# Performance work log

Hardware: AMD Instinct MI355X
Metric: run time of the kernel (lower is better)

## Reference

```python
import jax, jax.numpy as jnp
import numpy as np

B, L, H, W = 16, 4096, 64, 64
SEQ = 1024  # target_sequence_length (hardcoded in the torch module)
SP = 32     # sqrt(SEQ)


def _conv1d(x, w, b, pad):
    y = jax.lax.conv_general_dilated(x, w, (1,), [(pad, pad)],
                                     dimension_numbers=('NCH', 'OIH', 'NCH'))
    return y + b[None, :, None]


def _conv2d(x, w, b, pad, groups=1):
    y = jax.lax.conv_general_dilated(x, w, (1, 1), [(pad, pad)] * 2,
                                     feature_group_count=groups,
                                     dimension_numbers=('NCHW', 'OIHW', 'NCHW'))
    return y + b[None, :, None, None]


def _forward(us_input, img_input, us_w1, us_b1, us_w2, us_b2, us_w3, us_b3,
             aff_w, aff_w_high, aff_thr, img_w1, img_b1, img_w2, img_b2, img_w3, img_b3,
             db_qkv_w, db_qkv_b, db_dw_w, db_dw_b, db_proj_w, db_proj_b,
             db_fc_w, db_fc_b, db_dep_w, db_dep_b, db_temp,
             ca_qkv_w, ca_qkv_b, ca_out_w, ca_out_b,
             tf_ch1_w, tf_ch1_b, tf_ch2_w, tf_ch2_b,
             tf_sp1_w, tf_sp1_b, tf_sp2_w, tf_sp2_b, cls_w, cls_b):
    b = us_input.shape[0]
    # ---- ultrasound 1D conv branch ----
    x = us_input.transpose(0, 2, 1)                    # [B,1,L]
    x = jax.nn.relu(_conv1d(x, us_w1, us_b1, 1))
    x = jax.nn.relu(_conv1d(x, us_w2, us_b2, 1))
    x = jax.nn.relu(_conv1d(x, us_w3, us_b3, 1))
    us_feat = x.transpose(0, 2, 1)                     # [B,L,64]
    # ---- adaptive frequency filtering (training-mode high-freq mask included) ----
    n = us_feat.shape[1]
    xf = jnp.fft.rfft(us_feat, axis=1, norm='ortho')   # [B,Nf,64] complex
    w_c = aff_w[:, 0] + 1j * aff_w[:, 1]
    xw = xf * w_c
    energy = jnp.sum(jnp.abs(xf) ** 2, axis=-1)        # [B,Nf]
    med = jnp.median(energy.reshape(b, -1), axis=1, keepdims=True)
    ne = energy / (med + 1e-6)
    hard = (ne > aff_thr).astype(jnp.float32)
    mask = jax.lax.stop_gradient(hard - aff_thr) + aff_thr  # straight-through threshold
    wh_c = aff_w_high[:, 0] + 1j * aff_w_high[:, 1]
    xw = xw + (xf * mask[..., None]) * wh_c
    us_feat = jnp.fft.irfft(xw, n=n, axis=1, norm='ortho')  # [B,L,64]
    # ---- image 2D conv branch ----
    y = jax.nn.relu(_conv2d(img_input, img_w1, img_b1, 1))
    y = jax.nn.relu(_conv2d(y, img_w2, img_b2, 1))
    y = jax.nn.relu(_conv2d(y, img_w3, img_b3, 1))     # [B,64,H,W]
    # ---- dual-branch feature fusion block ----
    hgt, wid = y.shape[2], y.shape[3]
    hw = hgt * wid
    qkv = jnp.einsum('oi,bihw->bohw', db_qkv_w, y) + db_qkv_b[None, :, None, None]
    qkv = _conv2d(qkv, db_dw_w, db_dw_b, 1, groups=192)      # depthwise (3x3x3 conv @ D=1 -> center 3x3)
    # convolutional branch: faithful row-major reshape as in torch
    f_all = qkv.reshape(b, hw, 12, 16).transpose(0, 2, 1, 3)  # [B,12,HW,16]
    f_all = jnp.einsum('oi,bink->bonk', db_fc_w, f_all) + db_fc_b[None, :, None, None]
    f_conv = f_all.transpose(0, 3, 1, 2).reshape(b, 144, hgt, wid)
    out_conv = _conv2d(f_conv, db_dep_w, db_dep_b, 1, groups=16)  # [B,64,H,W]
    # channel attention branch
    q, k, v = jnp.split(qkv, 3, axis=1)
    q = q.reshape(b, 4, 16, hw)
    k = k.reshape(b, 4, 16, hw)
    v = v.reshape(b, 4, 16, hw)
    q = q / jnp.maximum(jnp.linalg.norm(q, axis=-1, keepdims=True), 1e-12)
    k = k / jnp.maximum(jnp.linalg.norm(k, axis=-1, keepdims=True), 1e-12)
    attn = jax.nn.softmax(jnp.einsum('bhcn,bhdn->bhcd', q, k) * db_temp, axis=-1)
    out = jnp.einsum('bhcd,bhdn->bhcn', attn, v).reshape(b, 64, hgt, wid)
    out = jnp.einsum('oi,bihw->bohw', db_proj_w, out) + db_proj_b[None, :, None, None]
    img_feat = (out + out_conv).reshape(b, 64, hw).transpose(0, 2, 1)  # [B,HW,64]
    # ---- adaptive avg pool to SEQ (lengths divide evenly) ----
    us_red = us_feat.transpose(0, 2, 1).reshape(b, 64, SEQ, -1).mean(-1).transpose(0, 2, 1)
    img_red = img_feat.transpose(0, 2, 1).reshape(b, 64, SEQ, -1).mean(-1).transpose(0, 2, 1)
    # ---- cross-modal attention (shared qkv/out projections) ----
    def heads(t):
        u = (jnp.einsum('bli,oi->blo', t, ca_qkv_w) + ca_qkv_b).reshape(b, SEQ, 4, 3, 16)
        return (u[:, :, :, 0].transpose(0, 2, 1, 3),
                u[:, :, :, 1].transpose(0, 2, 1, 3),
                u[:, :, :, 2].transpose(0, 2, 1, 3))
    q1, k1, v1 = heads(us_red)
    q2, k2, v2 = heads(img_red)
    scale = 1.0 / jnp.sqrt(jnp.float32(16.0))
    a1 = jax.nn.softmax(jnp.einsum('bhqd,bhkd->bhqk', q1, k2) * scale, axis=-1)
    a2 = jax.nn.softmax(jnp.einsum('bhqd,bhkd->bhqk', q2, k1) * scale, axis=-1)
    o1 = jnp.einsum('bhqk,bhkd->bhqd', a1, v2).transpose(0, 2, 1, 3).reshape(b, SEQ, 64)
    o2 = jnp.einsum('bhqk,bhkd->bhqd', a2, v1).transpose(0, 2, 1, 3).reshape(b, SEQ, 64)
    o1 = jnp.einsum('bli,oi->blo', o1, ca_out_w) + ca_out_b
    o2 = jnp.einsum('bli,oi->blo', o2, ca_out_w) + ca_out_b
    t1 = o1.transpose(0, 2, 1).reshape(b, 64, SP, SP)
    t2 = o2.transpose(0, 2, 1).reshape(b, 64, SP, SP)
    # ---- modal fusion attention (channel + spatial gating) ----
    ch_pool = jnp.stack([t1.mean((2, 3)), t1.max((2, 3)), t2.mean((2, 3)), t2.max((2, 3))], axis=1)  # [B,4,64]
    c1 = _conv1d(ch_pool, tf_ch1_w, tf_ch1_b, 1)      # [B,1,64]
    c2 = _conv1d(ch_pool, tf_ch2_w, tf_ch2_b, 1)
    ch_stack = jax.nn.softmax(jnp.stack([c1, c2], 0), axis=0)      # [2,B,1,64]
    ch_stack = ch_stack.transpose(0, 1, 3, 2)[..., None]           # [2,B,64,1,1]
    sp_pool = jnp.concatenate([t1.mean(1, keepdims=True), t1.max(1, keepdims=True),
                               t2.mean(1, keepdims=True), t2.max(1, keepdims=True)], axis=1)
    s1 = _conv2d(sp_pool, tf_sp1_w, tf_sp1_b, 3)
    s2 = _conv2d(sp_pool, tf_sp2_w, tf_sp2_b, 3)
    sp_stack = jax.nn.softmax(jnp.stack([s1, s2], 0), axis=0)      # [2,B,1,SP,SP]
    att = ch_stack + sp_stack + 1.0                                # [2,B,64,SP,SP]
    fuse = att[0] * t1 + att[1] * t2
    logits = fuse.mean((2, 3)) @ cls_w.T + cls_b
    return jax.nn.softmax(logits, axis=1)


def setup_inputs() -> dict:
    key = jax.random.key(0)
    ks = iter(jax.random.split(key, 64))
    def rn(shape, s=0.2):
        return jax.random.normal(next(ks), shape, dtype=jnp.float32) * s
    d = {
        'us_input': jax.random.normal(next(ks), (B, L, 1), dtype=jnp.float32),
        'img_input': jax.random.normal(next(ks), (B, 3, H, W), dtype=jnp.float32),
        'us_w1': rn((16, 1, 3)), 'us_b1': rn((16,), 0.02),
        'us_w2': rn((32, 16, 3)), 'us_b2': rn((32,), 0.02),
        'us_w3': rn((64, 32, 3)), 'us_b3': rn((64,), 0.02),
        'aff_w': rn((64, 2), 0.02), 'aff_w_high': rn((64, 2), 0.02),
        'aff_thr': jax.random.uniform(next(ks), (1,), dtype=jnp.float32),
        'img_w1': rn((16, 3, 3, 3)), 'img_b1': rn((16,), 0.02),
        'img_w2': rn((32, 16, 3, 3)), 'img_b2': rn((32,), 0.02),
        'img_w3': rn((64, 32, 3, 3)), 'img_b3': rn((64,), 0.02),
        'db_qkv_w': rn((192, 64), 0.1), 'db_qkv_b': rn((192,), 0.02),
        'db_dw_w': rn((192, 1, 3, 3)), 'db_dw_b': rn((192,), 0.02),
        'db_proj_w': rn((64, 64), 0.1), 'db_proj_b': rn((64,), 0.02),
        'db_fc_w': rn((9, 12), 0.1), 'db_fc_b': rn((9,), 0.02),
        'db_dep_w': rn((64, 9, 3, 3), 0.1), 'db_dep_b': rn((64,), 0.02),
        'db_temp': jnp.ones((4, 1, 1), dtype=jnp.float32),
        'ca_qkv_w': rn((192, 64), 0.1), 'ca_qkv_b': rn((192,), 0.02),
        'ca_out_w': rn((64, 64), 0.1), 'ca_out_b': rn((64,), 0.02),
        'tf_ch1_w': rn((1, 4, 3)), 'tf_ch1_b': rn((1,), 0.02),
        'tf_ch2_w': rn((1, 4, 3)), 'tf_ch2_b': rn((1,), 0.02),
        'tf_sp1_w': rn((1, 4, 7, 7)), 'tf_sp1_b': rn((1,), 0.02),
        'tf_sp2_w': rn((1, 4, 7, 7)), 'tf_sp2_b': rn((1,), 0.02),
        'cls_w': rn((9, 64), 0.1), 'cls_b': rn((9,), 0.02),
    }
    return d


def reference(us_input, img_input, us_w1, us_b1, us_w2, us_b2, us_w3, us_b3,
              aff_w, aff_w_high, aff_thr, img_w1, img_b1, img_w2, img_b2, img_w3, img_b3,
              db_qkv_w, db_qkv_b, db_dw_w, db_dw_b, db_proj_w, db_proj_b,
              db_fc_w, db_fc_b, db_dep_w, db_dep_b, db_temp,
              ca_qkv_w, ca_qkv_b, ca_out_w, ca_out_b,
              tf_ch1_w, tf_ch1_b, tf_ch2_w, tf_ch2_b,
              tf_sp1_w, tf_sp1_b, tf_sp2_w, tf_sp2_b, cls_w, cls_b):
    return _forward(us_input, img_input, us_w1, us_b1, us_w2, us_b2, us_w3, us_b3,
                    aff_w, aff_w_high, aff_thr, img_w1, img_b1, img_w2, img_b2, img_w3, img_b3,
                    db_qkv_w, db_qkv_b, db_dw_w, db_dw_b, db_proj_w, db_proj_b,
                    db_fc_w, db_fc_b, db_dep_w, db_dep_b, db_temp,
                    ca_qkv_w, ca_qkv_b, ca_out_w, ca_out_b,
                    tf_ch1_w, tf_ch1_b, tf_ch2_w, tf_ch2_b,
                    tf_sp1_w, tf_sp1_b, tf_sp2_w, tf_sp2_b, cls_w, cls_b)
```

## Files before the change

### kernel.cpp

```cpp
#include <hip/hip_runtime.h>

typedef float v2f __attribute__((ext_vector_type(2)));

static constexpr size_t O_SMALL   = 0;
static constexpr size_t O_US3     = 3145728;
static constexpr size_t O_XF      = 7340032;
static constexpr size_t O_USFILT  = 11536384;
static constexpr size_t O_ENERGY  = 15730688;
static constexpr size_t O_MED     = 15764480;
static constexpr size_t O_NRM     = 15765504;
static constexpr size_t O_ATTNS   = 15767552;
static constexpr size_t O_CHPOOL  = 15783936;
static constexpr size_t O_CHW     = 15788032;
static constexpr size_t O_SPPOOL  = 15790080;
static constexpr size_t O_SPW     = 15855616;
static constexpr size_t O_QKV     = 15888384;
static constexpr size_t O_QKVDW   = 28471296;
static constexpr size_t O_OUTCONV = 41054208;
static constexpr size_t CA_USRED = 0, CA_IMGRED = 1, CA_Q1 = 2, CA_K1 = 3, CA_V1 = 4,
                        CA_Q2 = 5, CA_K2 = 6, CA_V2 = 7, CA_O1 = 8, CA_O2 = 9,
                        CA_T1 = 10, CA_T2 = 11;

template<int Ci, int Co>
__global__ __launch_bounds__(256) void conv1d3_t(const float* __restrict__ in,
    const float* __restrict__ w, const float* __restrict__ bs, float* __restrict__ out)
{
    constexpr int T = 128;
    constexpr int G = 256 / Co;
    constexpr int N = T / G;
    __shared__ float lds[Ci][T + 2];
    int tid = threadIdx.x;
    int b  = blockIdx.x >> 5;
    int t0 = (blockIdx.x & 31) * T;
    const float* inb = in + (size_t)b * Ci * 4096;
    for (int i = tid; i < Ci * T; i += 256) {
        int ci = i / T, x = i % T;
        lds[ci][x + 1] = inb[ci * 4096 + t0 + x];
    }
    if (tid < Ci) {
        lds[tid][0]     = (t0 > 0)        ? inb[tid * 4096 + t0 - 1] : 0.f;
        lds[tid][T + 1] = (t0 + T < 4096) ? inb[tid * 4096 + t0 + T] : 0.f;
    }
    __syncthreads();
    int co = tid / G;
    int x0 = (tid % G) * N;
    float acc[N];
    float bias = bs[co];
#pragma unroll
    for (int j = 0; j < N; ++j) acc[j] = bias;
    const float* wb = w + co * Ci * 3;
    for (int ci = 0; ci < Ci; ++ci) {
        float w0 = wb[ci * 3], w1 = wb[ci * 3 + 1], w2 = wb[ci * 3 + 2];
        float a = lds[ci][x0], bb = lds[ci][x0 + 1];
#pragma unroll
        for (int j = 0; j < N; ++j) {
            float cc = lds[ci][x0 + 2 + j];
            acc[j] += w0 * a + w1 * bb + w2 * cc;
            a = bb; bb = cc;
        }
    }
    float* ob = out + ((size_t)b * Co + co) * 4096 + t0 + x0;
#pragma unroll
    for (int j = 0; j < N; ++j) ob[j] = fmaxf(acc[j], 0.f);
}

template<int Ci, int Co, int TY>
__global__ __launch_bounds__(256) void conv2d3_t(const float* __restrict__ in,
    const float* __restrict__ w, const float* __restrict__ bs, float* __restrict__ out)
{
    constexpr int G = 256 / (Co * TY);
    constexpr int N = 64 / G;
    __shared__ float lds[Ci][TY + 2][66];
    int tid = threadIdx.x;
    constexpr int NB = 64 / TY;
    int b  = blockIdx.x / NB;
    int y0 = (blockIdx.x % NB) * TY;
    const float* inb = in + (size_t)b * Ci * 4096;
    for (int i = tid; i < Ci * (TY + 2) * 64; i += 256) {
        int x  = i & 63;
        int ry = (i >> 6) % (TY + 2);
        int ci = i / ((TY + 2) * 64);
        int gy = y0 - 1 + ry;
        lds[ci][ry][x + 1] = (gy >= 0 && gy < 64) ? inb[ci * 4096 + gy * 64 + x] : 0.f;
    }
    for (int r = tid; r < Ci * (TY + 2); r += 256) {
        int ry = r % (TY + 2), ci = r / (TY + 2);
        lds[ci][ry][0] = 0.f; lds[ci][ry][65] = 0.f;
    }
    __syncthreads();
    int co   = tid / (TY * G);
    int ysub = (tid / G) % TY;
    int x0   = (tid % G) * N;
    float acc[N];
    float bias = bs[co];
#pragma unroll
    for (int j = 0; j < N; ++j) acc[j] = bias;
    const float* wb = w + co * Ci * 9;
    for (int ci = 0; ci < Ci; ++ci) {
        float wr[9];
#pragma unroll
        for (int k = 0; k < 9; ++k) wr[k] = wb[ci * 9 + k];
#pragma unroll
        for (int dy = 0; dy < 3; ++dy) {
            const float* lr = &lds[ci][ysub + dy][x0];
            float a = lr[0], bb = lr[1];
#pragma unroll
            for (int j = 0; j < N; ++j) {
                float cc = lr[2 + j];
                acc[j] += wr[dy * 3] * a + wr[dy * 3 + 1] * bb + wr[dy * 3 + 2] * cc;
// ... 13 lines not shown
    for (int s = 0; s < 6; ++s) {
        float cfac = -0.25f / (float)Ns;
        for (int r = 0; r < 4; ++r) {
            int j = (r << 8) + tid;
            float2 v0 = src[j];
            float2 v1 = src[j + 1024];
            float2 v2 = src[j + 2048];
            float2 v3 = src[j + 3072];
            int jm = j & (Ns - 1);
            float rev = (float)jm * cfac;
            float s1 = __builtin_amdgcn_sinf(rev);
            float c1 = __builtin_amdgcn_cosf(rev);
            float c2 = c1 * c1 - s1 * s1, s2 = 2.f * c1 * s1;
            float c3 = c2 * c1 - s2 * s1, s3 = c2 * s1 + s2 * c1;
            float2 u1 = make_float2(v1.x * c1 - v1.y * s1, v1.x * s1 + v1.y * c1);
            float2 u2 = make_float2(v2.x * c2 - v2.y * s2, v2.x * s2 + v2.y * c2);
            float2 u3 = make_float2(v3.x * c3 - v3.y * s3, v3.x * s3 + v3.y * c3);
            float t0x = v0.x + u2.x, t0y = v0.y + u2.y;
            float t1x = v0.x - u2.x, t1y = v0.y - u2.y;
            float t2x = u1.x + u3.x, t2y = u1.y + u3.y;
            float t3x = u1.x - u3.x, t3y = u1.y - u3.y;
            int base = ((j - jm) << 2) + jm;
            dst[base]          = make_float2(t0x + t2x, t0y + t2y);
            dst[base + Ns]     = make_float2(t1x + t3y, t1y - t3x);
            dst[base + 2 * Ns] = make_float2(t0x - t2x, t0y - t2y);
            dst[base + 3 * Ns] = make_float2(t1x - t3y, t1y + t3x);
        }
        __syncthreads();
        float2* tmp = src; src = dst; dst = tmp;
        Ns <<= 2;
    }
}

__global__ __launch_bounds__(256) void fft_fwd_kernel(const float* __restrict__ us3,
                                                      float* __restrict__ xf)
{
    __shared__ float2 A[4096];
    __shared__ float2 Bb[4096];
    int row = blockIdx.x;
    int tid = threadIdx.x;
    const float* x = us3 + (size_t)row * 4096;
    for (int r = 0; r < 16; ++r) {
        int i = (r << 8) + tid;
        A[i] = make_float2(x[i], 0.f);
    }
    __syncthreads();
    fft4096_r4(A, Bb, tid);
    float* out = xf + (size_t)row * 4098;
    for (int r = 0; r < 9; ++r) {
        int f = (r << 8) + tid;
        if (f < 2049) {
            out[2 * f]     = A[f].x * (1.f / 64.f);
            out[2 * f + 1] = A[f].y * (1.f / 64.f);
        }
    }
}

__global__ __launch_bounds__(256) void energy_kernel(const float* __restrict__ xf,
                                                     float* __restrict__ energy)
{
    int idx = blockIdx.x * 256 + threadIdx.x;
    if (idx >= 16 * 2049) return;
    int b = idx / 2049, f = idx % 2049;
    const float* p = xf + (size_t)b * 64 * 4098 + 2 * f;
    float e = 0.f;
    for (int ch = 0; ch < 64; ++ch) {
        float re = p[0], im = p[1];
        e += re * re + im * im;
        p += 4098;
    }
    energy[idx] = e;
}

__global__ __launch_bounds__(256) void median_kernel(const float* __restrict__ energy,
                                                     float* __restrict__ med)
{
    __shared__ float s[4096];
    int b = blockIdx.x;
    int tid = threadIdx.x;
    for (int r = 0; r < 16; ++r) {
        int i = (r << 8) + tid;
        s[i] = (i < 2049) ? energy[b * 2049 + i] : 3.0e38f;
    }
    __syncthreads();
    for (int k = 2; k <= 4096; k <<= 1) {
        for (int j = k >> 1; j > 0; j >>= 1) {
            for (int r = 0; r < 16; ++r) {
                int i = (r << 8) + tid;
                int ixj = i ^ j;
                if (ixj > i) {
                    bool up = ((i & k) == 0);
                    float a = s[i], bb = s[ixj];
                    if ((a > bb) == up) { s[i] = bb; s[ixj] = a; }
                }
            }
            __syncthreads();
        }
    }
    if (tid == 0) med[b] = s[1024];
}

__global__ __launch_bounds__(256) void filter_ifft_kernel(
    const float* __restrict__ xf, const float* __restrict__ energy, const float* __restrict__ med,
    const float* __restrict__ aff_w, const float* __restrict__ aff_wh, const float* __restrict__ thr_p,
    float* __restrict__ us_filt)
{
    __shared__ float2 A[4096];
    __shared__ float2 Bb[4096];
    int row = blockIdx.x;
    int b = row >> 6, ch = row & 63;
    int tid = threadIdx.x;
    float thr = thr_p[0];
    float mden = med[b] + 1e-6f;
    float w0r = aff_w[2 * ch], w0i = aff_w[2 * ch + 1];
    float whr = aff_wh[2 * ch], whi = aff_wh[2 * ch + 1];
    const float* X = xf + (size_t)row * 4098;
    const float* E = energy + b * 2049;
    for (int r = 0; r < 9; ++r) {
        int f = (r << 8) + tid;
        if (f < 2049) {
            float re = X[2 * f], im = X[2 * f + 1];
            float mask = (E[f] / mden > thr) ? 1.f : 0.f;
            float wr = w0r + mask * whr;
            float wi = w0i + mask * whi;
            float xr = re * wr - im * wi;
            float xi = re * wi + im * wr;
            A[f] = make_float2(xr, -xi);
            if (f >= 1 && f <= 2047) A[4096 - f] = make_float2(xr, xi);
        }
    }
    __syncthreads();
    fft4096_r4(A, Bb, tid);
    float* out = us_filt + (size_t)row * 4096;
    for (int r = 0; r < 16; ++r) {
        int i = (r << 8) + tid;
        out[i] = A[i].x * (1.f / 64.f);
    }
}

__global__ __launch_bounds__(256, 2) void qkv1x1_kernel(const float* __restrict__ y,
    const float* __restrict__ w, const float* __restrict__ bs, float* __restrict__ out)
{
    int blk = blockIdx.x;
    int oc = blk & 3;
    int pc = (blk >> 2) & 15;
    int b  = blk >> 6;
    int p = pc * 256 + threadIdx.x;
    const float* inb = y + (size_t)b * 262144 + p;
    v2f reg[32];
#pragma unroll
    for (int ci = 0; ci < 32; ++ci) {
        v2f r; r.x = inb[(2 * ci) * 4096]; r.y = inb[(2 * ci + 1) * 4096];
        reg[ci] = r;
    }
    float* ob = out + (size_t)b * 786432 + (size_t)oc * 48 * 4096 + p;
    for (int o = 0; o < 48; ++o) {
        const v2f* wr = (const v2f*)(w + (oc * 48 + o) * 64);
        v2f s2 = {0.f, 0.f};
#pragma unroll
        for (int ci = 0; ci < 32; ++ci) s2 = wr[ci] * reg[ci] + s2;
        ob[o * 4096] = bs[oc * 48 + o] + s2.x + s2.y;
    }
}

__global__ __launch_bounds__(256) void dwconv_kernel(const float* __restrict__ in,
    const float* __restrict__ w, const float* __restrict__ bs, float* __restrict__ out)
{
    int idx = blockIdx.x * 256 + threadIdx.x;
    int x = idx & 63, yy = (idx >> 6) & 63;
    int c = (idx >> 12) % 192;
    const float* p = in + idx;
    const float* wp = w + c * 9;
    float acc = bs[c];
    bool ym = yy > 0, yp = yy < 63, xm = x > 0, xp = x < 63;
    float s = wp[4] * p[0];
    if (ym) { s += wp[1] * p[-64]; if (xm) s += wp[0] * p[-65]; if (xp) s += wp[2] * p[-63]; }
    if (xm) s += wp[3] * p[-1];
    if (xp) s += wp[5] * p[1];
    if (yp) { s += wp[7] * p[64];  if (xm) s += wp[6] * p[63];  if (xp) s += wp[8] * p[65]; }
    out[idx] = acc + s;
}

__global__ __launch_bounds__(256) void fc_kernel(const float* __restrict__ qkv_dw,
    const float* __restrict__ fw, const float* __restrict__ fb, float* __restrict__ fcv)
{
    int idx = blockIdx.x * 256 + threadIdx.x;
    int k = idx & 15;
    int p = (idx >> 4) & 4095;
    int b = idx >> 16;
    const float* base = qkv_dw + (size_t)b * 786432;
    float u[12];
#pragma unroll
    for (int i = 0; i < 12; ++i) u[i] = base[p * 192 + i * 16 + k];
#pragma unroll
    for (int o = 0; o < 9; ++o) {
        float s = fb[o];
#pragma unroll
        for (int i = 0; i < 12; ++i) s += fw[o * 12 + i] * u[i];
        fcv[(((size_t)b * 16 + k) * 9 + o) * 4096 + p] = s;
    }
}

__global__ __launch_bounds__(256) void depconv2_kernel(const float* __restrict__ fcv,
    const float* __restrict__ w, const float* __restrict__ bs, float* __restrict__ out)
{
    __shared__ float lds[9][10][66];
    int blk = blockIdx.x;
    int band = blk & 7;
    int g    = (blk >> 3) & 15;
    int b    = blk >> 7;
    int y0 = band * 8;
    int tid = threadIdx.x;
    const float* inb = fcv + ((size_t)(b * 16 + g) * 9) * 4096;
    for (int i = tid; i < 9 * 10 * 64; i += 256) {
        int x  = i & 63;
        int ry = (i >> 6) % 10;
        int ci = i / 640;
        int gy = y0 - 1 + ry;
        lds[ci][ry][x + 1] = (gy >= 0 && gy < 64) ? inb[ci * 4096 + gy * 64 + x] : 0.f;
    }
    for (int i = tid; i < 90; i += 256) {
        int ry = i % 10, ci = i / 10;
        lds[ci][ry][0] = 0.f; lds[ci][ry][65] = 0.f;
    }
    __syncthreads();
    int co   = tid >> 6;
    int ysub = (tid >> 3) & 7;
    int x0   = (tid & 7) * 8;
    int ocg  = g * 4 + co;
    float acc[8];
    float bias = bs[ocg];
#pragma unroll
    for (int j = 0; j < 8; ++j) acc[j] = bias;
    const float* wb = w + ocg * 81;
    for (int ci = 0; ci < 9; ++ci) {
        float wr[9];
#pragma unroll
        for (int k = 0; k < 9; ++k) wr[k] = wb[ci * 9 + k];
#pragma unroll
        for (int dy = 0; dy < 3; ++dy) {
            const float* lr = &lds[ci][ysub + dy][x0];
            float a = lr[0], bb = lr[1];
#pragma unroll
            for (int j = 0; j < 8; ++j) {
                float cc = lr[2 + j];
                acc[j] += wr[dy * 3] * a + wr[dy * 3 + 1] * bb + wr[dy * 3 + 2] * cc;
                a = bb; bb = cc;
            }
        }
    }
    float* ob = out + ((size_t)b * 64 + ocg) * 4096 + (y0 + ysub) * 64 + x0;
#pragma unroll
    for (int j = 0; j < 8; ++j) ob[j] = acc[j];
}

__global__ __launch_bounds__(256) void qknorm_kernel(const float* __restrict__ qkv_dw,
                                                     float* __restrict__ nrm)
{
    int row = blockIdx.x;
    int which = row >> 10;
    int r = row & 1023;
    int b = r >> 6, hd = r & 63;
    const float* p = qkv_dw + ((size_t)b * 192 + which * 64 + hd) * 4096;
    float s = 0.f;
    for (int i = threadIdx.x; i < 4096; i += 256) { float v = p[i]; s += v * v; }
    __shared__ float red[256];
    red[threadIdx.x] = s;
    __syncthreads();
    for (int st = 128; st > 0; st >>= 1) {
        if (threadIdx.x < st) red[threadIdx.x] += red[threadIdx.x + st];
        __syncthreads();
    }
    if (threadIdx.x == 0) nrm[row] = sqrtf(red[0]);
}

__global__ __launch_bounds__(256) void chan_attn_kernel(
    const float* __restrict__ qkv_dw, const float* __restrict__ nrm,
    const float* __restrict__ temp, float* __restrict__ attn_s)
{
    int bh = blockIdx.x;
    int b = bh >> 2, h = bh & 3;
    __shared__ float Qs[16][130];
    __shared__ float Ks2[16][130];
    int c = threadIdx.x >> 4, d = threadIdx.x & 15;
    const float* qbase = qkv_dw + ((size_t)b * 192 + h * 16) * 4096;
    const float* kbase = qkv_dw + ((size_t)b * 192 + 64 + h * 16) * 4096;
    float s = 0.f;
    for (int n0 = 0; n0 < 4096; n0 += 128) {
        __syncthreads();
        for (int r = 0; r < 8; ++r) {
            int i = (r << 8) + threadIdx.x;
            int row = i >> 7, col = i & 127;
            Qs[row][col]  = qbase[(size_t)row * 4096 + n0 + col];
            Ks2[row][col] = kbase[(size_t)row * 4096 + n0 + col];
        }
        __syncthreads();
#pragma unroll 8
        for (int n = 0; n < 128; ++n) s += Qs[c][n] * Ks2[d][n];
    }
    float nq = fmaxf(nrm[b * 64 + h * 16 + c], 1e-12f);
    float nk = fmaxf(nrm[1024 + b * 64 + h * 16 + d], 1e-12f);
    s = s / (nq * nk) * temp[h];
    __shared__ float S[16][17];
    S[c][d] = s;
    __syncthreads();
    if (threadIdx.x < 16) {
        int cc = threadIdx.x;
// ... 229 lines not shown
    for (int d = 0; d < 16; ++d) {
        float s = 0.f;
#pragma unroll
        for (int i = 0; i < 4; ++i) s += accp[((size_t)(unit * 4 + i) * 1024 + q) * 16 + d];
        dst[d * 1024] = s * inv;
    }
}

__global__ __launch_bounds__(256, 2) void caout2_kernel(const float* __restrict__ o1t,
    const float* __restrict__ o2t, const float* __restrict__ ow, const float* __restrict__ ob_,
    float* __restrict__ t1, float* __restrict__ t2)
{
    int blk = blockIdx.x;
    int oc = blk & 1;
    int pc = (blk >> 1) & 3;
    int b  = (blk >> 3) & 15;
    int m  = blk >> 7;
    int l = pc * 256 + threadIdx.x;
    const float* in = (m ? o2t : o1t) + (size_t)b * 65536 + l;
    v2f reg[32];
#pragma unroll
    for (int i = 0; i < 32; ++i) {
        v2f r; r.x = in[(2 * i) * 1024]; r.y = in[(2 * i + 1) * 1024];
        reg[i] = r;
    }
    float* t = (m ? t2 : t1) + (size_t)b * 65536 + (size_t)oc * 32 * 1024 + l;
    for (int o = 0; o < 32; ++o) {
        const v2f* wr = (const v2f*)(ow + (oc * 32 + o) * 64);
        v2f s2 = {0.f, 0.f};
#pragma unroll
        for (int i = 0; i < 32; ++i) s2 = wr[i] * reg[i] + s2;
        t[o * 1024] = ob_[oc * 32 + o] + s2.x + s2.y;
    }
}

__global__ __launch_bounds__(256) void chpool2_kernel(const float* __restrict__ t1,
    const float* __restrict__ t2, float* __restrict__ chpool)
{
    int rg = blockIdx.x & 15;
    int b  = blockIdx.x >> 4;
    int wave = threadIdx.x >> 6, lane = threadIdx.x & 63;
    int c = rg * 4 + wave;
    const float* p1 = t1 + ((size_t)b * 64 + c) * 1024;
    const float* p2 = t2 + ((size_t)b * 64 + c) * 1024;
    float m1 = 0.f, x1 = -3e38f, m2 = 0.f, x2 = -3e38f;
#pragma unroll
    for (int i = 0; i < 16; ++i) {
        int p = lane + i * 64;
        float a = p1[p], bb = p2[p];
        m1 += a; x1 = fmaxf(x1, a);
        m2 += bb; x2 = fmaxf(x2, bb);
    }
    for (int off = 32; off > 0; off >>= 1) {
        m1 += __shfl_xor(m1, off);
        x1 = fmaxf(x1, __shfl_xor(x1, off));
        m2 += __shfl_xor(m2, off);
        x2 = fmaxf(x2, __shfl_xor(x2, off));
    }
    if (lane == 0) {
        chpool[b * 256 + c]       = m1 * (1.f / 1024.f);
        chpool[b * 256 + 64 + c]  = x1;
        chpool[b * 256 + 128 + c] = m2 * (1.f / 1024.f);
        chpool[b * 256 + 192 + c] = x2;
    }
}

__global__ __launch_bounds__(64) void chgate_kernel(const float* __restrict__ chpool,
    const float* __restrict__ w1, const float* __restrict__ b1,
    const float* __restrict__ w2, const float* __restrict__ b2, float* __restrict__ chw)
{
    int b = blockIdx.x, c = threadIdx.x;
    float a1 = b1[0], a2 = b2[0];
    for (int ic = 0; ic < 4; ++ic) {
        const float* cp = chpool + b * 256 + ic * 64;
        for (int d = -1; d <= 1; ++d) {
            int cc = c + d;
            if (cc >= 0 && cc < 64) {
                a1 += w1[ic * 3 + d + 1] * cp[cc];
                a2 += w2[ic * 3 + d + 1] * cp[cc];
            }
        }
    }
    float mx = fmaxf(a1, a2);
    float e1 = __expf(a1 - mx), e2 = __expf(a2 - mx);
    float inv = 1.f / (e1 + e2);
    chw[b * 64 + c]        = e1 * inv;
    chw[1024 + b * 64 + c] = e2 * inv;
}

__global__ __launch_bounds__(256) void sppool_kernel(const float* __restrict__ t1,
    const float* __restrict__ t2, float* __restrict__ sppool)
{
    int b = blockIdx.x >> 2;
    int p = (blockIdx.x & 3) * 256 + threadIdx.x;
    float m1 = 0.f, x1 = -3e38f, m2 = 0.f, x2 = -3e38f;
    const float* p1 = t1 + (size_t)b * 65536 + p;
    const float* p2 = t2 + (size_t)b * 65536 + p;
    for (int c = 0; c < 64; ++c) {
        float a = p1[c * 1024], bb = p2[c * 1024];
        m1 += a; x1 = fmaxf(x1, a);
        m2 += bb; x2 = fmaxf(x2, bb);
    }
    sppool[b * 4096 + p]        = m1 * (1.f / 64.f);
    sppool[b * 4096 + 1024 + p] = x1;
    sppool[b * 4096 + 2048 + p] = m2 * (1.f / 64.f);
    sppool[b * 4096 + 3072 + p] = x2;
}

__global__ __launch_bounds__(256) void spgate_kernel(const float* __restrict__ sppool,
    const float* __restrict__ w1, const float* __restrict__ b1,
    const float* __restrict__ w2, const float* __restrict__ b2, float* __restrict__ spw)
{
    int idx = blockIdx.x * 256 + threadIdx.x;
    int p = idx & 1023;
    int b = idx >> 10;
    int y = p >> 5, x = p & 31;
    float a1 = b1[0], a2 = b2[0];
    for (int ic = 0; ic < 4; ++ic) {
        const float* sp = sppool + b * 4096 + ic * 1024;
        for (int dy = -3; dy <= 3; ++dy) {
            int yy = y + dy;
            if (yy < 0 || yy > 31) continue;
            for (int dx = -3; dx <= 3; ++dx) {
                int xx = x + dx;
                if (xx < 0 || xx > 31) continue;
                float v = sp[yy * 32 + xx];
                int wi = ic * 49 + (dy + 3) * 7 + (dx + 3);
                a1 += w1[wi] * v;
                a2 += w2[wi] * v;
            }
        }
    }
    float mx = fmaxf(a1, a2);
    float e1 = __expf(a1 - mx), e2 = __expf(a2 - mx);
    float inv = 1.f / (e1 + e2);
    spw[idx]         = e1 * inv;
    spw[16384 + idx] = e2 * inv;
}

__global__ __launch_bounds__(256) void final2_kernel(const float* __restrict__ t1,
    const float* __restrict__ t2, const float* __restrict__ chw, const float* __restrict__ spw,
    const float* __restrict__ clsw, const float* __restrict__ clsb, float* __restrict__ out)
{
    int b = blockIdx.x;
    int wave = threadIdx.x >> 6, lane = threadIdx.x & 63;
    __shared__ float feat[64];
    __shared__ float lg[9];
    const float* s1 = spw + b * 1024;
    const float* s2 = spw + 16384 + b * 1024;
    for (int round = 0; round < 16; ++round) {
        int c = round * 4 + wave;
        float g1 = chw[b * 64 + c] + 1.f;
        float g2 = chw[1024 + b * 64 + c] + 1.f;
        const float* p1 = t1 + ((size_t)b * 64 + c) * 1024;
        const float* p2 = t2 + ((size_t)b * 64 + c) * 1024;
        float acc = 0.f;
#pragma unroll
        for (int i = 0; i < 16; ++i) {
            int p = lane + i * 64;
            acc += (g1 + s1[p]) * p1[p] + (g2 + s2[p]) * p2[p];
        }
        for (int off = 32; off > 0; off >>= 1) acc += __shfl_xor(acc, off);
        if (lane == 0) feat[c] = acc * (1.f / 1024.f);
    }
    __syncthreads();
    if (threadIdx.x < 9) {
        int c = threadIdx.x;
        float s = clsb[c];
        for (int i = 0; i < 64; ++i) s += clsw[c * 64 + i] * feat[i];
        lg[c] = s;
// ... 26 lines not shown
    const float* img_w2 = (const float*)d_in[13]; const float* img_b2 = (const float*)d_in[14];
    const float* img_w3 = (const float*)d_in[15]; const float* img_b3 = (const float*)d_in[16];
    const float* db_qkv_w = (const float*)d_in[17]; const float* db_qkv_b = (const float*)d_in[18];
    const float* db_dw_w = (const float*)d_in[19];  const float* db_dw_b = (const float*)d_in[20];
    const float* db_proj_w = (const float*)d_in[21]; const float* db_proj_b = (const float*)d_in[22];
    const float* db_fc_w = (const float*)d_in[23];  const float* db_fc_b = (const float*)d_in[24];
    const float* db_dep_w = (const float*)d_in[25]; const float* db_dep_b = (const float*)d_in[26];
    const float* db_temp = (const float*)d_in[27];
    const float* ca_qkv_w = (const float*)d_in[28]; const float* ca_qkv_b = (const float*)d_in[29];
    const float* ca_out_w = (const float*)d_in[30]; const float* ca_out_b = (const float*)d_in[31];
    const float* tf_ch1_w = (const float*)d_in[32]; const float* tf_ch1_b = (const float*)d_in[33];
    const float* tf_ch2_w = (const float*)d_in[34]; const float* tf_ch2_b = (const float*)d_in[35];
    const float* tf_sp1_w = (const float*)d_in[36]; const float* tf_sp1_b = (const float*)d_in[37];
    const float* tf_sp2_w = (const float*)d_in[38]; const float* tf_sp2_b = (const float*)d_in[39];
    const float* cls_w = (const float*)d_in[40];   const float* cls_b = (const float*)d_in[41];

    float* ws = (float*)d_ws;
    float* us1     = ws + O_SMALL;
    float* us2     = ws + O_SMALL + 1048576;
    float* us3     = ws + O_US3;
    float* xf      = ws + O_XF;
    float* us_filt = ws + O_USFILT;
    float* energy  = ws + O_ENERGY;
    float* med     = ws + O_MED;
    float* nrm     = ws + O_NRM;
    float* attn_s  = ws + O_ATTNS;
    float* chpool  = ws + O_CHPOOL;
    float* chw     = ws + O_CHW;
    float* sppool  = ws + O_SPPOOL;
    float* spw     = ws + O_SPW;
    float* qkv     = ws + O_QKV;
    float* qkv_dw  = ws + O_QKVDW;
    float* out_conv= ws + O_OUTCONV;
    float* img1 = us1, *img2 = us2;
    float* y = xf;
    float* fcv = qkv;
    float* img_feat = xf;
    float* us_redT  = ws + O_QKV + CA_USRED  * 1048576;
    float* img_redT = ws + O_QKV + CA_IMGRED * 1048576;
    float* q1 = ws + O_QKV + CA_Q1 * 1048576;
    float* k1 = ws + O_QKV + CA_K1 * 1048576;
    float* v1 = ws + O_QKV + CA_V1 * 1048576;
    float* q2 = ws + O_QKV + CA_Q2 * 1048576;
    float* k2 = ws + O_QKV + CA_K2 * 1048576;
    float* v2 = ws + O_QKV + CA_V2 * 1048576;
    float* o1t = ws + O_QKV + CA_O1 * 1048576;
    float* o2t = ws + O_QKV + CA_O2 * 1048576;
    float* t1 = ws + O_QKV + CA_T1 * 1048576;
    float* t2 = ws + O_QKV + CA_T2 * 1048576;
    float* ca_accp = ws + O_QKVDW;
    float* ca_ls   = ws + O_QKVDW + 8388608;
    float* ca_kmax = ws + O_QKVDW + 8912896;

    conv1d3_t<1, 16><<<512, 256, 0, stream>>>(us_input, us_w1, us_b1, us1);
    conv1d3_t<16, 32><<<512, 256, 0, stream>>>(us1, us_w2, us_b2, us2);
    conv1d3_t<32, 64><<<512, 256, 0, stream>>>(us2, us_w3, us_b3, us3);
    fft_fwd_kernel<<<1024, 256, 0, stream>>>(us3, xf);
    energy_kernel<<<129, 256, 0, stream>>>(xf, energy);
    median_kernel<<<16, 256, 0, stream>>>(energy, med);
    filter_ifft_kernel<<<1024, 256, 0, stream>>>(xf, energy, med, aff_w, aff_wh, aff_thr, us_filt);
    conv2d3_t<3, 16, 2><<<512, 256, 0, stream>>>(img_input, img_w1, img_b1, img1);
    conv2d3_t<16, 32, 2><<<512, 256, 0, stream>>>(img1, img_w2, img_b2, img2);
    conv2d3_t<32, 64, 2><<<512, 256, 0, stream>>>(img2, img_w3, img_b3, y);
    qkv1x1_kernel<<<1024, 256, 0, stream>>>(y, db_qkv_w, db_qkv_b, qkv);
    dwconv_kernel<<<49152, 256, 0, stream>>>(qkv, db_dw_w, db_dw_b, qkv_dw);
    fc_kernel<<<4096, 256, 0, stream>>>(qkv_dw, db_fc_w, db_fc_b, fcv);
    depconv2_kernel<<<2048, 256, 0, stream>>>(fcv, db_dep_w, db_dep_b, out_conv);
    qknorm_kernel<<<2048, 256, 0, stream>>>(qkv_dw, nrm);
    chan_attn_kernel<<<64, 256, 0, stream>>>(qkv_dw, nrm, db_temp, attn_s);
    attnproj_kernel<<<512, 256, 0, stream>>>(attn_s, qkv_dw, out_conv, db_proj_w, db_proj_b, img_feat);
    poolred_kernel<<<8192, 256, 0, stream>>>(us_filt, img_feat, us_redT, img_redT);
    caqkv2_kernel<<<512, 256, 0, stream>>>(us_redT, img_redT, ca_qkv_w, ca_qkv_b,
                                           q1, k1, v1, q2, k2, v2);
    kmax_kernel<<<128, 256, 0, stream>>>(k1, k2, ca_kmax);
    cross_attn6_kernel<<<512, 256, 0, stream>>>(q1, k1, v1, q2, k2, v2, ca_kmax, ca_ls, ca_accp);
    ca_merge2_kernel<<<512, 256, 0, stream>>>(ca_ls, ca_accp, o1t, o2t);
    caout2_kernel<<<256, 256, 0, stream>>>(o1t, o2t, ca_out_w, ca_out_b, t1, t2);
    chpool2_kernel<<<256, 256, 0, stream>>>(t1, t2, chpool);
    chgate_kernel<<<16, 64, 0, stream>>>(chpool, tf_ch1_w, tf_ch1_b, tf_ch2_w, tf_ch2_b, chw);
    sppool_kernel<<<64, 256, 0, stream>>>(t1, t2, sppool);
    spgate_kernel<<<64, 256, 0, stream>>>(sppool, tf_sp1_w, tf_sp1_b, tf_sp2_w, tf_sp2_b, spw);
    final2_kernel<<<16, 256, 0, stream>>>(t1, t2, chw, spw, cls_w, cls_b, (float*)d_out);
}
```

Measured before the change: 977.6 us.

## Merge independent ultrasound and image branch kernels into shared multi-role launches

Turns each kernel body into a device function and launches combined kernels whose block index picks which independent stage to run. The ultrasound and image branches, and the pooling and gate stages, now share launches. Workspace buffers are remapped so the merged stages do not alias each other. This is meant to cut launch count and fill idle compute units during small stages. The cost is that every merged kernel reserves the largest shared-memory footprint, and the FFT role's 64KB allocation can lower occupancy for the smaller roles.

New measurement: 988.0 us. No clear change (+1.1%).

```diff
diff --git a/kernel.cpp b/kernel.cpp
--- a/kernel.cpp
+++ b/kernel.cpp
@@ -21,17 +21,19 @@
                         CA_Q2 = 5, CA_K2 = 6, CA_V2 = 7, CA_O1 = 8, CA_O2 = 9,
                         CA_T1 = 10, CA_T2 = 11;
 
+
 template<int Ci, int Co>
-__global__ __launch_bounds__(256) void conv1d3_t(const float* __restrict__ in,
-    const float* __restrict__ w, const float* __restrict__ bs, float* __restrict__ out)
+__device__ __forceinline__ void conv1d3_body(char* smem_raw, int bid,
+    const float* __restrict__ in, const float* __restrict__ w,
+    const float* __restrict__ bs, float* __restrict__ out)
 {
     constexpr int T = 128;
     constexpr int G = 256 / Co;
     constexpr int N = T / G;
-    __shared__ float lds[Ci][T + 2];
+    auto lds = (float(*)[T + 2])smem_raw;
     int tid = threadIdx.x;
-    int b  = blockIdx.x >> 5;
-    int t0 = (blockIdx.x & 31) * T;
+    int b  = bid >> 5;
+    int t0 = (bid & 31) * T;
     const float* inb = in + (size_t)b * Ci * 4096;
     for (int i = tid; i < Ci * T; i += 256) {
         int ci = i / T, x = i % T;
@@ -65,16 +67,17 @@
 }
 
 template<int Ci, int Co, int TY>
-__global__ __launch_bounds__(256) void conv2d3_t(const float* __restrict__ in,
-    const float* __restrict__ w, const float* __restrict__ bs, float* __restrict__ out)
+__device__ __forceinline__ void conv2d3_body(char* smem_raw, int bid,
+    const float* __restrict__ in, const float* __restrict__ w,
+    const float* __restrict__ bs, float* __restrict__ out)
 {
     constexpr int G = 256 / (Co * TY);
     constexpr int N = 64 / G;
-    __shared__ float lds[Ci][TY + 2][66];
+    auto lds = (float(*)[TY + 2][66])smem_raw;
     int tid = threadIdx.x;
     constexpr int NB = 64 / TY;
-    int b  = blockIdx.x / NB;
-    int y0 = (blockIdx.x % NB) * TY;
+    int b  = bid / NB;
+    int y0 = (bid % NB) * TY;
     const float* inb = in + (size_t)b * Ci * 4096;
     for (int i = tid; i < Ci * (TY + 2) * 64; i += 256) {
         int x  = i & 63;
@@ -154,12 +157,11 @@
     }
 }
 
-__global__ __launch_bounds__(256) void fft_fwd_kernel(const float* __restrict__ us3,
-                                                      float* __restrict__ xf)
-{
-    __shared__ float2 A[4096];
-    __shared__ float2 Bb[4096];
-    int row = blockIdx.x;
+__device__ __forceinline__ void fft_fwd_body(char* smem_raw, int row,
+    const float* __restrict__ us3, float* __restrict__ xf)
+{
+    float2* A  = (float2*)smem_raw;
+    float2* Bb = A + 4096;
     int tid = threadIdx.x;
     const float* x = us3 + (size_t)row * 4096;
     for (int r = 0; r < 16; ++r) {
@@ -178,10 +180,10 @@
     }
 }
 
-__global__ __launch_bounds__(256) void energy_kernel(const float* __restrict__ xf,
-                                                     float* __restrict__ energy)
-{
-    int idx = blockIdx.x * 256 + threadIdx.x;
+__device__ __forceinline__ void energy_body(int bid,
+    const float* __restrict__ xf, float* __restrict__ energy)
+{
+    int idx = bid * 256 + threadIdx.x;
     if (idx >= 16 * 2049) return;
     int b = idx / 2049, f = idx % 2049;
     const float* p = xf + (size_t)b * 64 * 4098 + 2 * f;
@@ -194,11 +196,10 @@
     energy[idx] = e;
 }
 
-__global__ __launch_bounds__(256) void median_kernel(const float* __restrict__ energy,
-                                                     float* __restrict__ med)
-{
-    __shared__ float s[4096];
-    int b = blockIdx.x;
+__device__ __forceinline__ void median_body(char* smem_raw, int b,
+    const float* __restrict__ energy, float* __restrict__ med)
+{
+    float* s = (float*)smem_raw;
     int tid = threadIdx.x;
     for (int r = 0; r < 16; ++r) {
         int i = (r << 8) + tid;
@@ -222,14 +223,14 @@
     if (tid == 0) med[b] = s[1024];
 }
 
-__global__ __launch_bounds__(256) void filter_ifft_kernel(
-    const float* __restrict__ xf, const float* __restrict__ energy, const float* __restrict__ med,
-    const float* __restrict__ aff_w, const float* __restrict__ aff_wh, const float* __restrict__ thr_p,
+__device__ __forceinline__ void filter_ifft_body(char* smem_raw, int row,
+    const float* __restrict__ xf, const float* __restrict__ energy,
+    const float* __restrict__ med, const float* __restrict__ aff_w,
+    const float* __restrict__ aff_wh, const float* __restrict__ thr_p,
     float* __restrict__ us_filt)
 {
-    __shared__ float2 A[4096];
-    __shared__ float2 Bb[4096];
-    int row = blockIdx.x;
+    float2* A  = (float2*)smem_raw;
+    float2* Bb = A + 4096;
     int b = row >> 6, ch = row & 63;
     int tid = threadIdx.x;
     float thr = thr_p[0];
@@ -260,13 +261,12 @@
     }
 }
 
-__global__ __launch_bounds__(256, 2) void qkv1x1_kernel(const float* __restrict__ y,
+__device__ __forceinline__ void qkv1x1_body(int bid, const float* __restrict__ y,
     const float* __restrict__ w, const float* __restrict__ bs, float* __restrict__ out)
 {
-    int blk = blockIdx.x;
-    int oc = blk & 3;
-    int pc = (blk >> 2) & 15;
-    int b  = blk >> 6;
+    int oc = bid & 3;
+    int pc = (bid >> 2) & 15;
+    int b  = bid >> 6;
     int p = pc * 256 + threadIdx.x;
     const float* inb = y + (size_t)b * 262144 + p;
     v2f reg[32];
@@ -285,10 +285,10 @@
     }
 }
 
-__global__ __launch_bounds__(256) void dwconv_kernel(const float* __restrict__ in,
+__device__ __forceinline__ void dwconv_body(int bid, const float* __restrict__ in,
     const float* __restrict__ w, const float* __restrict__ bs, float* __restrict__ out)
 {
-    int idx = blockIdx.x * 256 + threadIdx.x;
+    int idx = bid * 256 + threadIdx.x;
     int x = idx & 63, yy = (idx >> 6) & 63;
     int c = (idx >> 12) % 192;
     const float* p = in + idx;
@@ -303,10 +303,10 @@
     out[idx] = acc + s;
 }
 
-__global__ __launch_bounds__(256) void fc_kernel(const float* __restrict__ qkv_dw,
+__device__ __forceinline__ void fc_body(int bid, const float* __restrict__ qkv_dw,
     const float* __restrict__ fw, const float* __restrict__ fb, float* __restrict__ fcv)
 {
-    int idx = blockIdx.x * 256 + threadIdx.x;
+    int idx = bid * 256 + threadIdx.x;
     int k = idx & 15;
     int p = (idx >> 4) & 4095;
     int b = idx >> 16;
@@ -323,14 +323,14 @@
     }
 }
 
-__global__ __launch_bounds__(256) void depconv2_kernel(const float* __restrict__ fcv,
-    const float* __restrict__ w, const float* __restrict__ bs, float* __restrict__ out)
-{
-    __shared__ float lds[9][10][66];
-    int blk = blockIdx.x;
-    int band = blk & 7;
-    int g    = (blk >> 3) & 15;
-    int b    = blk >> 7;
+__device__ __forceinline__ void depconv2_body(char* smem_raw, int bid,
+    const float* __restrict__ fcv, const float* __restrict__ w,
+    const float* __restrict__ bs, float* __restrict__ out)
+{
+    auto lds = (float(*)[10][66])smem_raw;
+    int band = bid & 7;
+    int g    = (bid >> 3) & 15;
+    int b    = bid >> 7;
     int y0 = band * 8;
     int tid = threadIdx.x;
     const float* inb = fcv + ((size_t)(b * 16 + g) * 9) * 4096;
@@ -376,17 +376,16 @@
     for (int j = 0; j < 8; ++j) ob[j] = acc[j];
 }
 
-__global__ __launch_bounds__(256) void qknorm_kernel(const float* __restrict__ qkv_dw,
-                                                     float* __restrict__ nrm)
-{
-    int row = blockIdx.x;
+__device__ __forceinline__ void qknorm_body(char* smem_raw, int row,
+    const float* __restrict__ qkv_dw, float* __restrict__ nrm)
+{
+    float* red = (float*)smem_raw;
     int which = row >> 10;
     int r = row & 1023;
     int b = r >> 6, hd = r & 63;
     const float* p = qkv_dw + ((size_t)b * 192 + which * 64 + hd) * 4096;
     float s = 0.f;
     for (int i = threadIdx.x; i < 4096; i += 256) { float v = p[i]; s += v * v; }
-    __shared__ float red[256];
     red[threadIdx.x] = s;
     __syncthreads();
     for (int st = 128; st > 0; st >>= 1) {
@@ -395,6 +394,187 @@
     }
     if (threadIdx.x == 0) nrm[row] = sqrtf(red[0]);
 }
+
+__device__ __forceinline__ void chpool2_body(int bid, const float* __restrict__ t1,
+    const float* __restrict__ t2, float* __restrict__ chpool)
+{
+    int rg = bid & 15;
+    int b  = bid >> 4;
+    int wave = threadIdx.x >> 6, lane = threadIdx.x & 63;
+    int c = rg * 4 + wave;
+    const float* p1 = t1 + ((size_t)b * 64 + c) * 1024;
+    const float* p2 = t2 + ((size_t)b * 64 + c) * 1024;
+    float m1 = 0.f, x1 = -3e38f, m2 = 0.f, x2 = -3e38f;
+#pragma unroll
+    for (int i = 0; i < 16; ++i) {
+        int p = lane + i * 64;
+        float a = p1[p], bb = p2[p];
+        m1 += a; x1 = fmaxf(x1, a);
+        m2 += bb; x2 = fmaxf(x2, bb);
+    }
+    for (int off = 32; off > 0; off >>= 1) {
+        m1 += __shfl_xor(m1, off);
+        x1 = fmaxf(x1, __shfl_xor(x1, off));
+        m2 += __shfl_xor(m2, off);
+        x2 = fmaxf(x2, __shfl_xor(x2, off));
+    }
+    if (lane == 0) {
+        chpool[b * 256 + c]       = m1 * (1.f / 1024.f);
+        chpool[b * 256 + 64 + c]  = x1;
+        chpool[b * 256 + 128 + c] = m2 * (1.f / 1024.f);
+        chpool[b * 256 + 192 + c] = x2;
+    }
+}
+
+__device__ __forceinline__ void sppool_body(int bid, const float* __restrict__ t1,
+    const float* __restrict__ t2, float* __restrict__ sppool)
+{
+    int b = bid >> 2;
+    int p = (bid & 3) * 256 + threadIdx.x;
+    float m1 = 0.f, x1 = -3e38f, m2 = 0.f, x2 = -3e38f;
+    const float* p1 = t1 + (size_t)b * 65536 + p;
+    const float* p2 = t2 + (size_t)b * 65536 + p;
+    for (int c = 0; c < 64; ++c) {
+        float a = p1[c * 1024], bb = p2[c * 1024];
+        m1 += a; x1 = fmaxf(x1, a);
+        m2 += bb; x2 = fmaxf(x2, bb);
+    }
+    sppool[b * 4096 + p]        = m1 * (1.f / 64.f);
+    sppool[b * 4096 + 1024 + p] = x1;
+    sppool[b * 4096 + 2048 + p] = m2 * (1.f / 64.f);
+    sppool[b * 4096 + 3072 + p] = x2;
+}
+
+__device__ __forceinline__ void chgate_body(int b, const float* __restrict__ chpool,
+    const float* __restrict__ w1, const float* __restrict__ b1,
+    const float* __restrict__ w2, const float* __restrict__ b2, float* __restrict__ chw)
+{
+    int c = threadIdx.x;
+    if (c >= 64) return;
+    float a1 = b1[0], a2 = b2[0];
+    for (int ic = 0; ic < 4; ++ic) {
+        const float* cp = chpool + b * 256 + ic * 64;
+        for (int d = -1; d <= 1; ++d) {
+            int cc = c + d;
+            if (cc >= 0 && cc < 64) {
+                a1 += w1[ic * 3 + d + 1] * cp[cc];
+                a2 += w2[ic * 3 + d + 1] * cp[cc];
+            }
+        }
+    }
+    float mx = fmaxf(a1, a2);
+    float e1 = __expf(a1 - mx), e2 = __expf(a2 - mx);
+    float inv = 1.f / (e1 + e2);
+    chw[b * 64 + c]        = e1 * inv;
+    chw[1024 + b * 64 + c] = e2 * inv;
+}
+
+__device__ __forceinline__ void spgate_body(int bid, const float* __restrict__ sppool,
+    const float* __restrict__ w1, const float* __restrict__ b1,
+    const float* __restrict__ w2, const float* __restrict__ b2, float* __restrict__ spw)
+{
+    int idx = bid * 256 + threadIdx.x;
+    int p = idx & 1023;
+    int b = idx >> 10;
+    int y = p >> 5, x = p & 31;
+    float a1 = b1[0], a2 = b2[0];
+    for (int ic = 0; ic < 4; ++ic) {
+        const float* sp = sppool + b * 4096 + ic * 1024;
+        for (int dy = -3; dy <= 3; ++dy) {
+            int yy = y + dy;
+            if (yy < 0 || yy > 31) continue;
+            for (int dx = -3; dx <= 3; ++dx) {
+                int xx = x + dx;
+                if (xx < 0 || xx > 31) continue;
+                float v = sp[yy * 32 + xx];
+                int wi = ic * 49 + (dy + 3) * 7 + (dx + 3);
+                a1 += w1[wi] * v;
+                a2 += w2[wi] * v;
+            }
+        }
+    }
+    float mx = fmaxf(a1, a2);
+    float e1 = __expf(a1 - mx), e2 = __expf(a2 - mx);
+    float inv = 1.f / (e1 + e2);
+    spw[idx]         = e1 * inv;
+    spw[16384 + idx] = e2 * inv;
+}
+
+
+__global__ __launch_bounds__(256) void s1_kernel(const float* us_in, const float* uw, const float* ub,
+    float* uo, const float* iin, const float* iw, const float* ib, float* io)
+{
+    __shared__ __align__(16) char smem[3168];
+    if (blockIdx.x < 512) conv1d3_body<1, 16>(smem, blockIdx.x, us_in, uw, ub, uo);
+    else                  conv2d3_body<3, 16, 2>(smem, blockIdx.x - 512, iin, iw, ib, io);
+}
+
+__global__ __launch_bounds__(256) void s2_kernel(const float* ui, const float* uw, const float* ub,
+    float* uo, const float* ii, const float* iw, const float* ib, float* io)
+{
+    __shared__ __align__(16) char smem[16896];
+    if (blockIdx.x < 512) conv1d3_body<16, 32>(smem, blockIdx.x, ui, uw, ub, uo);
+    else                  conv2d3_body<16, 32, 2>(smem, blockIdx.x - 512, ii, iw, ib, io);
+}
+
+__global__ __launch_bounds__(256) void s3_kernel(const float* ui, const float* uw, const float* ub,
+    float* uo, const float* ii, const float* iw, const float* ib, float* io)
+{
+    __shared__ __align__(16) char smem[33792];
+    if (blockIdx.x < 512) conv1d3_body<32, 64>(smem, blockIdx.x, ui, uw, ub, uo);
+    else                  conv2d3_body<32, 64, 2>(smem, blockIdx.x - 512, ii, iw, ib, io);
+}
+
+__global__ __launch_bounds__(256) void s4_kernel(const float* us3, float* xf,
+    const float* y, const float* qw, const float* qb, float* qkv)
+{
+    __shared__ __align__(16) char smem[65536];
+    if (blockIdx.x < 1024) fft_fwd_body(smem, blockIdx.x, us3, xf);
+    else                   qkv1x1_body(blockIdx.x - 1024, y, qw, qb, qkv);
+}
+
+__global__ __launch_bounds__(256) void s5_kernel(const float* qkv, const float* dww,
+    const float* dwb, float* qkv_dw, const float* xf, float* energy)
+{
+    if (blockIdx.x < 49152) dwconv_body(blockIdx.x, qkv, dww, dwb, qkv_dw);
+    else                    energy_body(blockIdx.x - 49152, xf, energy);
+}
+
+__global__ __launch_bounds__(256) void s6_kernel(const float* qkv_dw, const float* fw,
+    const float* fb, float* fcv, const float* energy, float* med)
+{
+    __shared__ __align__(16) char smem[16384];
+    if (blockIdx.x < 4096) fc_body(blockIdx.x, qkv_dw, fw, fb, fcv);
+    else                   median_body(smem, blockIdx.x - 4096, energy, med);
+}
+
+__global__ __launch_bounds__(256) void s7_kernel(const float* fcv, const float* dw,
+    const float* db, float* out_conv, const float* qkv_dw, float* nrm,
+    const float* xf, const float* energy, const float* med, const float* aw,
+    const float* awh, const float* thr, float* us_filt)
+{
+    __shared__ __align__(16) char smem[65536];
+    if (blockIdx.x < 2048)      depconv2_body(smem, blockIdx.x, fcv, dw, db, out_conv);
+    else if (blockIdx.x < 4096) qknorm_body(smem, blockIdx.x - 2048, qkv_dw, nrm);
+    else                        filter_ifft_body(smem, blockIdx.x - 4096, xf, energy, med, aw, awh, thr, us_filt);
+}
+
+__global__ __launch_bounds__(256) void s16_kernel(const float* t1, const float* t2,
+    float* chpool, float* sppool)
+{
+    if (blockIdx.x < 256) chpool2_body(blockIdx.x, t1, t2, chpool);
+    else                  sppool_body(blockIdx.x - 256, t1, t2, sppool);
+}
+
+__global__ __launch_bounds__(256) void s17_kernel(const float* sppool, const float* sw1,
+    const float* sb1, const float* sw2, const float* sb2, float* spw,
+    const float* chpool, const float* cw1, const float* cb1, const float* cw2,
+    const float* cb2, float* chw)
+{
+    if (blockIdx.x < 64) spgate_body(blockIdx.x, sppool, sw1, sb1, sw2, sb2, spw);
+    else                 chgate_body(blockIdx.x - 64, chpool, cw1, cb1, cw2, cb2, chw);
+}
+
 
 __global__ __launch_bounds__(256) void chan_attn_kernel(
     const float* __restrict__ qkv_dw, const float* __restrict__ nrm,
@@ -690,110 +870,6 @@
         for (int i = 0; i < 32; ++i) s2 = wr[i] * reg[i] + s2;
         t[o * 1024] = ob_[oc * 32 + o] + s2.x + s2.y;
     }
-}
-
-__global__ __launch_bounds__(256) void chpool2_kernel(const float* __restrict__ t1,
-    const float* __restrict__ t2, float* __restrict__ chpool)
-{
-    int rg = blockIdx.x & 15;
-    int b  = blockIdx.x >> 4;
-    int wave = threadIdx.x >> 6, lane = threadIdx.x & 63;
-    int c = rg * 4 + wave;
-    const float* p1 = t1 + ((size_t)b * 64 + c) * 1024;
-    const float* p2 = t2 + ((size_t)b * 64 + c) * 1024;
-    float m1 = 0.f, x1 = -3e38f, m2 = 0.f, x2 = -3e38f;
-#pragma unroll
-    for (int i = 0; i < 16; ++i) {
-        int p = lane + i * 64;
-        float a = p1[p], bb = p2[p];
-        m1 += a; x1 = fmaxf(x1, a);
-        m2 += bb; x2 = fmaxf(x2, bb);
-    }
-    for (int off = 32; off > 0; off >>= 1) {
-        m1 += __shfl_xor(m1, off);
-        x1 = fmaxf(x1, __shfl_xor(x1, off));
-        m2 += __shfl_xor(m2, off);
-        x2 = fmaxf(x2, __shfl_xor(x2, off));
-    }
-    if (lane == 0) {
-        chpool[b * 256 + c]       = m1 * (1.f / 1024.f);
-        chpool[b * 256 + 64 + c]  = x1;
-        chpool[b * 256 + 128 + c] = m2 * (1.f / 1024.f);
-        chpool[b * 256 + 192 + c] = x2;
-    }
-}
-
-__global__ __launch_bounds__(64) void chgate_kernel(const float* __restrict__ chpool,
-    const float* __restrict__ w1, const float* __restrict__ b1,
-    const float* __restrict__ w2, const float* __restrict__ b2, float* __restrict__ chw)
-{
-    int b = blockIdx.x, c = threadIdx.x;
-    float a1 = b1[0], a2 = b2[0];
-    for (int ic = 0; ic < 4; ++ic) {
-        const float* cp = chpool + b * 256 + ic * 64;
-        for (int d = -1; d <= 1; ++d) {
-            int cc = c + d;
-            if (cc >= 0 && cc < 64) {
-                a1 += w1[ic * 3 + d + 1] * cp[cc];
-                a2 += w2[ic * 3 + d + 1] * cp[cc];
-            }
-        }
-    }
-    float mx = fmaxf(a1, a2);
-    float e1 = __expf(a1 - mx), e2 = __expf(a2 - mx);
-    float inv = 1.f / (e1 + e2);
-    chw[b * 64 + c]        = e1 * inv;
-    chw[1024 + b * 64 + c] = e2 * inv;
-}
-
-__global__ __launch_bounds__(256) void sppool_kernel(const float* __restrict__ t1,
-    const float* __restrict__ t2, float* __restrict__ sppool)
-{
-    int b = blockIdx.x >> 2;
-    int p = (blockIdx.x & 3) * 256 + threadIdx.x;
-    float m1 = 0.f, x1 = -3e38f, m2 = 0.f, x2 = -3e38f;
-    const float* p1 = t1 + (size_t)b * 65536 + p;
-    const float* p2 = t2 + (size_t)b * 65536 + p;
-    for (int c = 0; c < 64; ++c) {
-        float a = p1[c * 1024], bb = p2[c * 1024];
-        m1 += a; x1 = fmaxf(x1, a);
-        m2 += bb; x2 = fmaxf(x2, bb);
-    }
-    sppool[b * 4096 + p]        = m1 * (1.f / 64.f);
-    sppool[b * 4096 + 1024 + p] = x1;
-    sppool[b * 4096 + 2048 + p] = m2 * (1.f / 64.f);
-    sppool[b * 4096 + 3072 + p] = x2;
-}
-
-__global__ __launch_bounds__(256) void spgate_kernel(const float* __restrict__ sppool,
-    const float* __restrict__ w1, const float* __restrict__ b1,
-    const float* __restrict__ w2, const float* __restrict__ b2, float* __restrict__ spw)
-{
-    int idx = blockIdx.x * 256 + threadIdx.x;
-    int p = idx & 1023;
-    int b = idx >> 10;
-    int y = p >> 5, x = p & 31;
-    float a1 = b1[0], a2 = b2[0];
-    for (int ic = 0; ic < 4; ++ic) {
-        const float* sp = sppool + b * 4096 + ic * 1024;
-        for (int dy = -3; dy <= 3; ++dy) {
-            int yy = y + dy;
-            if (yy < 0 || yy > 31) continue;
-            for (int dx = -3; dx <= 3; ++dx) {
-                int xx = x + dx;
-                if (xx < 0 || xx > 31) continue;
-                float v = sp[yy * 32 + xx];
-                int wi = ic * 49 + (dy + 3) * 7 + (dx + 3);
-                a1 += w1[wi] * v;
-                a2 += w2[wi] * v;
-            }
-        }
-    }
-    float mx = fmaxf(a1, a2);
-    float e1 = __expf(a1 - mx), e2 = __expf(a2 - mx);
-    float inv = 1.f / (e1 + e2);
-    spw[idx]         = e1 * inv;
-    spw[16384 + idx] = e2 * inv;
 }
 
 __global__ __launch_bounds__(256) void final2_kernel(const float* __restrict__ t1,
@@ -886,8 +962,9 @@
     float* qkv     = ws + O_QKV;
     float* qkv_dw  = ws + O_QKVDW;
     float* out_conv= ws + O_OUTCONV;
-    float* img1 = us1, *img2 = us2;
-    float* y = xf;
+    float* img1 = ws + O_USFILT;
+    float* img2 = ws + O_USFILT + 1048576;
+    float* y = ws + O_QKVDW;
     float* fcv = qkv;
     float* img_feat = xf;
     float* us_redT  = ws + O_QKV + CA_USRED  * 1048576;
@@ -906,21 +983,18 @@
     float* ca_ls   = ws + O_QKVDW + 8388608;
     float* ca_kmax = ws + O_QKVDW + 8912896;
 
-    conv1d3_t<1, 16><<<512, 256, 0, stream>>>(us_input, us_w1, us_b1, us1);
-    conv1d3_t<16, 32><<<512, 256, 0, stream>>>(us1, us_w2, us_b2, us2);
-    conv1d3_t<32, 64><<<512, 256, 0, stream>>>(us2, us_w3, us_b3, us3);
-    fft_fwd_kernel<<<1024, 256, 0, stream>>>(us3, xf);
-    energy_kernel<<<129, 256, 0, stream>>>(xf, energy);
-    median_kernel<<<16, 256, 0, stream>>>(energy, med);
-    filter_ifft_kernel<<<1024, 256, 0, stream>>>(xf, energy, med, aff_w, aff_wh, aff_thr, us_filt);
-    conv2d3_t<3, 16, 2><<<512, 256, 0, stream>>>(img_input, img_w1, img_b1, img1);
-    conv2d3_t<16, 32, 2><<<512, 256, 0, stream>>>(img1, img_w2, img_b2, img2);
-    conv2d3_t<32, 64, 2><<<512, 256, 0, stream>>>(img2, img_w3, img_b3, y);
-    qkv1x1_kernel<<<1024, 256, 0, stream>>>(y, db_qkv_w, db_qkv_b, qkv);
-    dwconv_kernel<<<49152, 256, 0, stream>>>(qkv, db_dw_w, db_dw_b, qkv_dw);
-    fc_kernel<<<4096, 256, 0, stream>>>(qkv_dw, db_fc_w, db_fc_b, fcv);
-    depconv2_kernel<<<2048, 256, 0, stream>>>(fcv, db_dep_w, db_dep_b, out_conv);
-    qknorm_kernel<<<2048, 256, 0, stream>>>(qkv_dw, nrm);
+    s1_kernel<<<1024, 256, 0, stream>>>(us_input, us_w1, us_b1, us1,
+                                        img_input, img_w1, img_b1, img1);
+    s2_kernel<<<1024, 256, 0, stream>>>(us1, us_w2, us_b2, us2,
+                                        img1, img_w2, img_b2, img2);
+    s3_kernel<<<1024, 256, 0, stream>>>(us2, us_w3, us_b3, us3,
+                                        img2, img_w3, img_b3, y);
+    s4_kernel<<<2048, 256, 0, stream>>>(us3, xf, y, db_qkv_w, db_qkv_b, qkv);
+    s5_kernel<<<49281, 256, 0, stream>>>(qkv, db_dw_w, db_dw_b, qkv_dw, xf, energy);
+    s6_kernel<<<4112, 256, 0, stream>>>(qkv_dw, db_fc_w, db_fc_b, fcv, energy, med);
+    s7_kernel<<<5120, 256, 0, stream>>>(fcv, db_dep_w, db_dep_b, out_conv,
+                                        qkv_dw, nrm, xf, energy, med,
+                                        aff_w, aff_wh, aff_thr, us_filt);
     chan_attn_kernel<<<64, 256, 0, stream>>>(qkv_dw, nrm, db_temp, attn_s);
     attnproj_kernel<<<512, 256, 0, stream>>>(attn_s, qkv_dw, out_conv, db_proj_w, db_proj_b, img_feat);
     poolred_kernel<<<8192, 256, 0, stream>>>(us_filt, img_feat, us_redT, img_redT);
@@ -930,9 +1004,8 @@
     cross_attn6_kernel<<<512, 256, 0, stream>>>(q1, k1, v1, q2, k2, v2, ca_kmax, ca_ls, ca_accp);
     ca_merge2_kernel<<<512, 256, 0, stream>>>(ca_ls, ca_accp, o1t, o2t);
     caout2_kernel<<<256, 256, 0, stream>>>(o1t, o2t, ca_out_w, ca_out_b, t1, t2);
-    chpool2_kernel<<<256, 256, 0, stream>>>(t1, t2, chpool);
-    chgate_kernel<<<16, 64, 0, stream>>>(chpool, tf_ch1_w, tf_ch1_b, tf_ch2_w, tf_ch2_b, chw);
-    sppool_kernel<<<64, 256, 0, stream>>>(t1, t2, sppool);
-    spgate_kernel<<<64, 256, 0, stream>>>(sppool, tf_sp1_w, tf_sp1_b, tf_sp2_w, tf_sp2_b, spw);
+    s16_kernel<<<320, 256, 0, stream>>>(t1, t2, chpool, sppool);
+    s17_kernel<<<80, 256, 0, stream>>>(sppool, tf_sp1_w, tf_sp1_b, tf_sp2_w, tf_sp2_b, spw,
+                                       chpool, tf_ch1_w, tf_ch1_b, tf_ch2_w, tf_ch2_b, chw);
     final2_kernel<<<16, 256, 0, stream>>>(t1, t2, chw, spw, cls_w, cls_b, (float*)d_out);
 }
```
